# Performance work log

Hardware: AMD Instinct MI355X
Metric: run time of the kernel (lower is better)

The kernel has to match this reference:

```python
import jax, jax.numpy as jnp
import numpy as np

DIM = 256
HEADS = 8
HEAD_DIM = DIM // HEADS
SCALE = HEAD_DIM ** -0.5
EPS = 1e-6


def setup_inputs() -> dict:
    key = jax.random.key(0)
    k1, k2 = jax.random.split(key)
    feat = jax.random.normal(k1, (8, DIM, 40, 40), dtype=jnp.float32)
    ln_w = jnp.ones((DIM,), dtype=jnp.float32)
    ln_b = jnp.zeros((DIM,), dtype=jnp.float32)
    qkv_w = jax.random.normal(k2, (3 * DIM, DIM), dtype=jnp.float32) * 0.02  # trunc_normal std=0.02 approx
    qkv_b = jnp.zeros((3 * DIM,), dtype=jnp.float32)
    return {"feat": feat, "ln_w": ln_w, "ln_b": ln_b, "qkv_w": qkv_w, "qkv_b": qkv_b}


def _layernorm(x, w, b):
    mu = jnp.mean(x, axis=-1, keepdims=True)
    var = jnp.mean((x - mu) ** 2, axis=-1, keepdims=True)
    return (x - mu) * jax.lax.rsqrt(var + EPS) * w + b


def reference(feat, ln_w, ln_b, qkv_w, qkv_b):
    b, c, h, w = feat.shape
    T = h * w
    tokens = feat.reshape(b, c, T).transpose(0, 2, 1)  # (B, T, C)
    tokens = _layernorm(tokens, ln_w, ln_b)
    qkv = tokens @ qkv_w.T + qkv_b                     # (B, T, 3C)
    qkv = qkv.reshape(b, T, 3, HEADS, HEAD_DIM).transpose(2, 0, 3, 1, 4)  # (3, B, H, T, d)
    q, k = qkv[0], qkv[1]
    scores = jnp.einsum('bhtd,bhsd->bhts', q, k) * SCALE  # (B, H, T, T)
    attn = jax.nn.softmax(scores, axis=-1)
    return attn
```

## Files before the change

kernel.cpp:

```cpp
#include <hip/hip_runtime.h>
#include <math.h>

#define DIM 256
#define HEADS 8
#define HD 32
#define T 1600
#define B 8
#define NBH (B * HEADS)
#define SCALE 0.17677669529663687f
#define EPS 1e-6f

__global__ __launch_bounds__(256) void transpose_w(const float* __restrict__ W,
                                                   float* __restrict__ Wt) {
    int idx = blockIdx.x * 256 + threadIdx.x;
    int r = idx & 511;
    int c = idx >> 9;
    Wt[c * 512 + r] = W[r * 256 + c];
}

#define TOK 32
__global__ __launch_bounds__(256) void ln_qkv(const float* __restrict__ feat,
                                              const float* __restrict__ lnw,
                                              const float* __restrict__ lnb,
                                              const float* __restrict__ qkvb,
                                              const float* __restrict__ Wt,
                                              float* __restrict__ qws,
                                              float* __restrict__ ktws) {
    __shared__ float x[DIM * TOK];
    __shared__ float red[2][8][TOK];
    __shared__ float mus[TOK], rstd[TOK];

    const int tid = threadIdx.x;
    const int blk = blockIdx.x;
    const int b = blk / (T / TOK);
    const int t0 = (blk % (T / TOK)) * TOK;
    const int tp = tid & 31;
    const int g = tid >> 5;

    const float* fb = feat + (size_t)b * DIM * T + t0;

    for (int cc = 0; cc < DIM; cc += 8) {
        int c = cc + g;
        x[c * TOK + tp] = fb[(size_t)c * T + tp];
    }
    __syncthreads();

    float s = 0.f, sq = 0.f;
    for (int i = 0; i < 32; ++i) {
        float v = x[(g * 32 + i) * TOK + tp];
        s += v;
        sq += v * v;
    }
    red[0][g][tp] = s;
    red[1][g][tp] = sq;
    __syncthreads();
    if (tid < TOK) {
        float ts = 0.f, tq = 0.f;
        for (int i = 0; i < 8; ++i) { ts += red[0][i][tid]; tq += red[1][i][tid]; }
        float mu = ts * (1.f / DIM);
        float var = tq * (1.f / DIM) - mu * mu;
        mus[tid] = mu;
        rstd[tid] = rsqrtf(var + EPS);
    }
    __syncthreads();

    for (int cc = 0; cc < DIM; cc += 8) {
        int c = cc + g;
        float w = lnw[c];
        float bb = lnb[c];
        float v = x[c * TOK + tp];
        x[c * TOK + tp] = (v - mus[tp]) * rstd[tp] * w + bb;
    }
    __syncthreads();

    float accq[TOK], acck[TOK];
#pragma unroll
    for (int t = 0; t < TOK; ++t) { accq[t] = 0.f; acck[t] = 0.f; }

    for (int c = 0; c < DIM; ++c) {
        float wq = Wt[c * 512 + tid];
        float wk = Wt[c * 512 + 256 + tid];
        const float* xr = &x[c * TOK];
#pragma unroll
        for (int t = 0; t < TOK; ++t) {
            float xv = xr[t];
            accq[t] += wq * xv;
            acck[t] += wk * xv;
        }
    }

    const float bq = qkvb[tid];
    const float bk = qkvb[256 + tid];
    const int h = tid >> 5;
    const int d = tid & 31;

    float* qp = qws + ((size_t)(b * HEADS + h) * T + t0) * HD + d;
#pragma unroll
    for (int t = 0; t < TOK; ++t) qp[(size_t)t * HD] = (accq[t] + bq) * SCALE;

    float* kp = ktws + ((size_t)(b * HEADS + h) * HD + d) * T + t0;
#pragma unroll
    for (int t = 0; t < TOK; ++t) kp[t] = acck[t] + bk;
}

#define ROWS 8
#define JJ 7
__global__ __launch_bounds__(256) void attn_softmax(const float* __restrict__ qws,
                                                    const float* __restrict__ ktws,
                                                    float* __restrict__ out) {
    __shared__ float qs[HD][ROWS];
    __shared__ float redm[4][ROWS], redl[4][ROWS];

    const int tid = threadIdx.x;
    const int blk = blockIdx.x;
    const int bh = blk / (T / ROWS);
    const int r0 = (blk % (T / ROWS)) * ROWS;

    {
        int i = tid >> 5, d = tid & 31;
        qs[d][i] = qws[((size_t)bh * T + r0 + i) * HD + d];
    }
    __syncthreads();

    float acc[ROWS][JJ];
#pragma unroll
    for (int i = 0; i < ROWS; ++i)
#pragma unroll
        for (int jj = 0; jj < JJ; ++jj) acc[i][jj] = 0.f;

    const bool v6 = tid < (T - 6 * 256);
    const float* kb = ktws + (size_t)bh * HD * T;

    for (int d = 0; d < HD; ++d) {
        const float4* q4 = (const float4*)&qs[d][0];
        float4 qa = q4[0];
        float4 qb = q4[1];
        const float* kr = kb + d * T;
#pragma unroll
        for (int jj = 0; jj < JJ; ++jj) {
            int j = tid + jj * 256;
            float kv = (jj < 6 || v6) ? kr[j < T ? j : 0] : 0.f;
            acc[0][jj] += qa.x * kv;
            acc[1][jj] += qa.y * kv;
            acc[2][jj] += qa.z * kv;
            acc[3][jj] += qa.w * kv;
            acc[4][jj] += qb.x * kv;
            acc[5][jj] += qb.y * kv;
            acc[6][jj] += qb.z * kv;
            acc[7][jj] += qb.w * kv;
        }
    }

    const int w = tid >> 6;
    const int lane = tid & 63;

#pragma unroll
    for (int i = 0; i < ROWS; ++i) {
        float v = -3e38f;
#pragma unroll
        for (int jj = 0; jj < 6; ++jj) v = fmaxf(v, acc[i][jj]);
        if (v6) v = fmaxf(v, acc[i][6]);
#pragma unroll
        for (int off = 32; off; off >>= 1) v = fmaxf(v, __shfl_xor(v, off, 64));
        if (lane == 0) redm[w][i] = v;
    }
    __syncthreads();
    float m[ROWS];
#pragma unroll
    for (int i = 0; i < ROWS; ++i)
        m[i] = fmaxf(fmaxf(redm[0][i], redm[1][i]), fmaxf(redm[2][i], redm[3][i]));
    __syncthreads();

#pragma unroll
    for (int i = 0; i < ROWS; ++i) {
        float s = 0.f;
#pragma unroll
        for (int jj = 0; jj < JJ; ++jj) {
            float p = __expf(acc[i][jj] - m[i]);
            if (jj == 6 && !v6) p = 0.f;
            acc[i][jj] = p;
            s += p;
        }
#pragma unroll
        for (int off = 32; off; off >>= 1) s += __shfl_xor(s, off, 64);
        if (lane == 0) redl[w][i] = s;
    }
    __syncthreads();
    float rinv[ROWS];
#pragma unroll
    for (int i = 0; i < ROWS; ++i)
        rinv[i] = 1.0f / (redl[0][i] + redl[1][i] + redl[2][i] + redl[3][i]);

    float* ob = out + (size_t)bh * T * T + (size_t)r0 * T;
#pragma unroll
    for (int i = 0; i < ROWS; ++i) {
#pragma unroll
        for (int jj = 0; jj < JJ; ++jj) {
            int j = tid + jj * 256;
            if (jj < 6 || v6) ob[(size_t)i * T + j] = acc[i][jj] * rinv[i];
        }
    }
}

extern "C" void kernel_launch(void* const* d_in, const int* in_sizes, int n_in,
                              void* d_out, int out_size, void* d_ws, size_t ws_size,
                              hipStream_t stream) {
    const float* feat = (const float*)d_in[0];
    const float* lnw = (const float*)d_in[1];
    const float* lnb = (const float*)d_in[2];
    const float* qkvw = (const float*)d_in[3];
    const float* qkvb = (const float*)d_in[4];
    float* out = (float*)d_out;

    float* Wt = (float*)d_ws;
    float* qws = Wt + 256 * 512;
    float* ktws = qws + (size_t)NBH * T * HD;

    transpose_w<<<512, 256, 0, stream>>>(qkvw, Wt);
    ln_qkv<<<(B * T) / TOK, 256, 0, stream>>>(feat, lnw, lnb, qkvb, Wt, qws, ktws);
    attn_softmax<<<NBH * (T / ROWS), 256, 0, stream>>>(qws, ktws, out);
}
```

Before: 868.9 us.

## Vectorize attention-softmax column tiles as float4 and halve ln_qkv token tile

The attention kernel now gives each thread two float4 column groups instead of seven scalar strided columns. K loads and the 8x1600 output stores become 128-bit accesses, with the next d-row of K prefetched into registers. The ln_qkv kernel uses 16-token tiles for more blocks, loads feat with float4, prefetches the next weight row, and writes K with float4 stores. Costs include extra prefetch registers, a launch_bounds occupancy hint, and a g1 branch that leaves part of the block idle on the second column group.

```diff
diff --git a/kernel.cpp b/kernel.cpp
--- a/kernel.cpp
+++ b/kernel.cpp
@@ -18,7 +18,7 @@
     Wt[c * 512 + r] = W[r * 256 + c];
 }
 
-#define TOK 32
+#define TOK 16
 __global__ __launch_bounds__(256) void ln_qkv(const float* __restrict__ feat,
                                               const float* __restrict__ lnw,
                                               const float* __restrict__ lnb,
@@ -27,27 +27,35 @@
                                               float* __restrict__ qws,
                                               float* __restrict__ ktws) {
     __shared__ float x[DIM * TOK];
-    __shared__ float red[2][8][TOK];
+    __shared__ float red[2][16][TOK];
     __shared__ float mus[TOK], rstd[TOK];
 
     const int tid = threadIdx.x;
     const int blk = blockIdx.x;
     const int b = blk / (T / TOK);
     const int t0 = (blk % (T / TOK)) * TOK;
-    const int tp = tid & 31;
-    const int g = tid >> 5;
 
     const float* fb = feat + (size_t)b * DIM * T + t0;
 
-    for (int cc = 0; cc < DIM; cc += 8) {
-        int c = cc + g;
-        x[c * TOK + tp] = fb[(size_t)c * T + tp];
-    }
-    __syncthreads();
+    {
+        const int c0 = tid >> 2;
+        const int t4 = (tid & 3) * 4;
+#pragma unroll
+        for (int p = 0; p < 4; ++p) {
+            int c = c0 + p * 64;
+            float4 v = *(const float4*)(fb + (size_t)c * T + t4);
+            *(float4*)&x[c * TOK + t4] = v;
+        }
+    }
+    __syncthreads();
+
+    const int g = tid >> 4;
+    const int tp = tid & 15;
 
     float s = 0.f, sq = 0.f;
-    for (int i = 0; i < 32; ++i) {
-        float v = x[(g * 32 + i) * TOK + tp];
+#pragma unroll
+    for (int i = 0; i < 16; ++i) {
+        float v = x[(g * 16 + i) * TOK + tp];
         s += v;
         sq += v * v;
     }
@@ -56,7 +64,8 @@
     __syncthreads();
     if (tid < TOK) {
         float ts = 0.f, tq = 0.f;
-        for (int i = 0; i < 8; ++i) { ts += red[0][i][tid]; tq += red[1][i][tid]; }
+#pragma unroll
+        for (int i = 0; i < 16; ++i) { ts += red[0][i][tid]; tq += red[1][i][tid]; }
         float mu = ts * (1.f / DIM);
         float var = tq * (1.f / DIM) - mu * mu;
         mus[tid] = mu;
@@ -64,12 +73,11 @@
     }
     __syncthreads();
 
-    for (int cc = 0; cc < DIM; cc += 8) {
-        int c = cc + g;
-        float w = lnw[c];
-        float bb = lnb[c];
+#pragma unroll
+    for (int i = 0; i < 16; ++i) {
+        int c = g * 16 + i;
         float v = x[c * TOK + tp];
-        x[c * TOK + tp] = (v - mus[tp]) * rstd[tp] * w + bb;
+        x[c * TOK + tp] = (v - mus[tp]) * rstd[tp] * lnw[c] + lnb[c];
     }
     __syncthreads();
 
@@ -77,16 +85,21 @@
 #pragma unroll
     for (int t = 0; t < TOK; ++t) { accq[t] = 0.f; acck[t] = 0.f; }
 
+    float wq = Wt[tid];
+    float wk = Wt[256 + tid];
     for (int c = 0; c < DIM; ++c) {
-        float wq = Wt[c * 512 + tid];
-        float wk = Wt[c * 512 + 256 + tid];
+        const int cn = (c + 1) & 255;
+        float wqn = Wt[cn * 512 + tid];
+        float wkn = Wt[cn * 512 + 256 + tid];
         const float* xr = &x[c * TOK];
 #pragma unroll
         for (int t = 0; t < TOK; ++t) {
             float xv = xr[t];
-            accq[t] += wq * xv;
-            acck[t] += wk * xv;
-        }
+            accq[t] = fmaf(wq, xv, accq[t]);
+            acck[t] = fmaf(wk, xv, acck[t]);
+        }
+        wq = wqn;
+        wk = wkn;
     }
 
     const float bq = qkvb[tid];
@@ -100,14 +113,21 @@
 
     float* kp = ktws + ((size_t)(b * HEADS + h) * HD + d) * T + t0;
 #pragma unroll
-    for (int t = 0; t < TOK; ++t) kp[t] = acck[t] + bk;
+    for (int tt = 0; tt < TOK / 4; ++tt) {
+        float4 v;
+        v.x = acck[4 * tt + 0] + bk;
+        v.y = acck[4 * tt + 1] + bk;
+        v.z = acck[4 * tt + 2] + bk;
+        v.w = acck[4 * tt + 3] + bk;
+        ((float4*)kp)[tt] = v;
+    }
 }
 
 #define ROWS 8
-#define JJ 7
-__global__ __launch_bounds__(256) void attn_softmax(const float* __restrict__ qws,
-                                                    const float* __restrict__ ktws,
-                                                    float* __restrict__ out) {
+#define NT4 (T / 4)
+__global__ __launch_bounds__(256, 4) void attn_softmax(const float* __restrict__ qws,
+                                                       const float* __restrict__ ktws,
+                                                       float* __restrict__ out) {
     __shared__ float qs[HD][ROWS];
     __shared__ float redm[4][ROWS], redl[4][ROWS];
 
@@ -122,82 +142,108 @@
     }
     __syncthreads();
 
-    float acc[ROWS][JJ];
+    float acc0[ROWS][4], acc1[ROWS][4];
 #pragma unroll
     for (int i = 0; i < ROWS; ++i)
 #pragma unroll
-        for (int jj = 0; jj < JJ; ++jj) acc[i][jj] = 0.f;
-
-    const bool v6 = tid < (T - 6 * 256);
-    const float* kb = ktws + (size_t)bh * HD * T;
+        for (int j = 0; j < 4; ++j) { acc0[i][j] = 0.f; acc1[i][j] = 0.f; }
+
+    const bool g1 = tid < (NT4 - 256);
+    const int i1 = g1 ? 256 + tid : tid;
+    const float4* kb4 = (const float4*)(ktws + (size_t)bh * HD * T);
+
+    float4 kv0 = kb4[tid];
+    float4 kv1 = kb4[i1];
 
     for (int d = 0; d < HD; ++d) {
         const float4* q4 = (const float4*)&qs[d][0];
         float4 qa = q4[0];
         float4 qb = q4[1];
-        const float* kr = kb + d * T;
-#pragma unroll
-        for (int jj = 0; jj < JJ; ++jj) {
-            int j = tid + jj * 256;
-            float kv = (jj < 6 || v6) ? kr[j < T ? j : 0] : 0.f;
-            acc[0][jj] += qa.x * kv;
-            acc[1][jj] += qa.y * kv;
-            acc[2][jj] += qa.z * kv;
-            acc[3][jj] += qa.w * kv;
-            acc[4][jj] += qb.x * kv;
-            acc[5][jj] += qb.y * kv;
-            acc[6][jj] += qb.z * kv;
-            acc[7][jj] += qb.w * kv;
-        }
+        const int dn = (d + 1) & 31;
+        float4 nk0 = kb4[dn * NT4 + tid];
+        float4 nk1 = kb4[dn * NT4 + i1];
+
+        float qv[8] = {qa.x, qa.y, qa.z, qa.w, qb.x, qb.y, qb.z, qb.w};
+#pragma unroll
+        for (int i = 0; i < ROWS; ++i) {
+            acc0[i][0] = fmaf(qv[i], kv0.x, acc0[i][0]);
+            acc0[i][1] = fmaf(qv[i], kv0.y, acc0[i][1]);
+            acc0[i][2] = fmaf(qv[i], kv0.z, acc0[i][2]);
+            acc0[i][3] = fmaf(qv[i], kv0.w, acc0[i][3]);
+        }
+        if (g1) {
+#pragma unroll
+            for (int i = 0; i < ROWS; ++i) {
+                acc1[i][0] = fmaf(qv[i], kv1.x, acc1[i][0]);
+                acc1[i][1] = fmaf(qv[i], kv1.y, acc1[i][1]);
+                acc1[i][2] = fmaf(qv[i], kv1.z, acc1[i][2]);
+                acc1[i][3] = fmaf(qv[i], kv1.w, acc1[i][3]);
+            }
+        }
+        kv0 = nk0;
+        kv1 = nk1;
     }
 
     const int w = tid >> 6;
     const int lane = tid & 63;
 
+    float m[ROWS];
 #pragma unroll
     for (int i = 0; i < ROWS; ++i) {
-        float v = -3e38f;
-#pragma unroll
-        for (int jj = 0; jj < 6; ++jj) v = fmaxf(v, acc[i][jj]);
-        if (v6) v = fmaxf(v, acc[i][6]);
+        float v = fmaxf(fmaxf(acc0[i][0], acc0[i][1]), fmaxf(acc0[i][2], acc0[i][3]));
+        if (g1) {
+            float v1 = fmaxf(fmaxf(acc1[i][0], acc1[i][1]), fmaxf(acc1[i][2], acc1[i][3]));
+            v = fmaxf(v, v1);
+        }
 #pragma unroll
         for (int off = 32; off; off >>= 1) v = fmaxf(v, __shfl_xor(v, off, 64));
         if (lane == 0) redm[w][i] = v;
     }
     __syncthreads();
-    float m[ROWS];
 #pragma unroll
     for (int i = 0; i < ROWS; ++i)
         m[i] = fmaxf(fmaxf(redm[0][i], redm[1][i]), fmaxf(redm[2][i], redm[3][i]));
-    __syncthreads();
 
 #pragma unroll
     for (int i = 0; i < ROWS; ++i) {
         float s = 0.f;
 #pragma unroll
-        for (int jj = 0; jj < JJ; ++jj) {
-            float p = __expf(acc[i][jj] - m[i]);
-            if (jj == 6 && !v6) p = 0.f;
-            acc[i][jj] = p;
+        for (int j = 0; j < 4; ++j) {
+            float p = __expf(acc0[i][j] - m[i]);
+            acc0[i][j] = p;
             s += p;
+        }
+        if (g1) {
+#pragma unroll
+            for (int j = 0; j < 4; ++j) {
+                float p = __expf(acc1[i][j] - m[i]);
+                acc1[i][j] = p;
+                s += p;
+            }
         }
 #pragma unroll
         for (int off = 32; off; off >>= 1) s += __shfl_xor(s, off, 64);
         if (lane == 0) redl[w][i] = s;
     }
     __syncthreads();
-    float rinv[ROWS];
-#pragma unroll
-    for (int i = 0; i < ROWS; ++i)
-        rinv[i] = 1.0f / (redl[0][i] + redl[1][i] + redl[2][i] + redl[3][i]);
 
     float* ob = out + (size_t)bh * T * T + (size_t)r0 * T;
 #pragma unroll
     for (int i = 0; i < ROWS; ++i) {
-#pragma unroll
-        for (int jj = 0; jj < JJ; ++jj) {
-            int j = tid + jj * 256;
-            if (jj < 6 || v6) ob[(size_t)i * T + j] = acc[i][jj] * rinv[i];
+        float rinv = 1.0f / ((redl[0][i] + redl[1][i]) + (redl[2][i] + redl[3][i]));
+        float4 o;
+        o.x = acc0[i][0] * rinv;
+        o.y = acc0[i][1] * rinv;
+        o.z = acc0[i][2] * rinv;
+        o.w = acc0[i][3] * rinv;
+        ((float4*)(ob + (size_t)i * T))[tid] = o;
+        if (g1) {
+            float4 o1;
+            o1.x = acc1[i][0] * rinv;
+            o1.y = acc1[i][1] * rinv;
+            o1.z = acc1[i][2] * rinv;
+            o1.w = acc1[i][3] * rinv;
+            ((float4*)(ob + (size_t)i * T))[256 + tid] = o1;
         }
     }
 }
```

Result: no change. 866.1 us (-0.3%).
